# Performance work log

Measured on AMD Instinct MI355X. Metric: run time of the kernel, lower is better.

## Reference

```python
import jax, jax.numpy as jnp
import numpy as np

B, N, D, E_PER, NT, ET, L = 32, 64, 128, 512, 32, 16, 6
E = B * E_PER


def _ln(y, g, b, eps=1e-5):
    m = jnp.mean(y, -1, keepdims=True)
    v = jnp.mean((y - m) ** 2, -1, keepdims=True)
    return (y - m) * jax.lax.rsqrt(v + eps) * g + b


def setup_inputs() -> dict:
    key = jax.random.key(0)
    ks = jax.random.split(key, 40)
    x = jax.random.randint(ks[0], (B * N,), 0, NT)
    src = jax.random.randint(ks[1], (E,), 0, N)
    dst = jax.random.randint(ks[2], (E,), 0, N)
    off = jnp.repeat(jnp.arange(B) * N, E_PER)
    edge_index = jnp.stack([src + off, dst + off])
    edge_attr = jax.random.randint(ks[3], (E,), 0, ET)
    t = jax.random.uniform(ks[4], (B,))

    def lin(k, fi, fo):
        return jax.random.normal(k, (fi, fo), jnp.float32) / np.sqrt(fi).astype(np.float32)

    inp = {
        'x': x, 'edge_index': edge_index, 'edge_attr': edge_attr, 't': t,
        'node_emb': (jax.random.normal(ks[5], (NT, D)) * 0.02).at[0].set(0.0),
        'edge_emb': (jax.random.normal(ks[6], (ET, D)) * 0.02).at[0].set(0.0),
        'temb_W1': lin(ks[7], 1, D), 'temb_b1': jnp.zeros(D),
        'temb_W2': lin(ks[8], D, D), 'temb_b2': jnp.zeros(D),
        'nin_W1': lin(ks[9], D, 2 * D), 'nin_b1': jnp.zeros(2 * D),
        'nin_W2': lin(ks[10], 2 * D, D), 'nin_b2': jnp.zeros(D),
        'ein_W1': lin(ks[11], D, 2 * D), 'ein_b1': jnp.zeros(2 * D),
        'ein_W2': lin(ks[12], 2 * D, D), 'ein_b2': jnp.zeros(D),
        'conv_W1': jax.random.normal(ks[13], (L, 3 * D, D)) / np.sqrt(3 * D).astype(np.float32),
        'conv_b1': jnp.zeros((L, D)),
        'conv_g1': jnp.ones((L, D)), 'conv_bt1': jnp.zeros((L, D)),
        'conv_W2': jax.random.normal(ks[14], (L, D, D)) / np.sqrt(D).astype(np.float32),
        'conv_b2': jnp.zeros((L, D)),
        'conv_g2': jnp.ones((L, D)), 'conv_bt2': jnp.zeros((L, D)),
        'mlp_W1': lin(ks[15], D, D), 'mlp_b1': jnp.zeros(D),
        'mlp_W2': lin(ks[16], D, D), 'mlp_b2': jnp.zeros(D),
        'fn_W1': lin(ks[17], D, 2 * D), 'fn_b1': jnp.zeros(2 * D),
        'fn_W2': lin(ks[18], 2 * D, D), 'fn_b2': jnp.zeros(D),
    }
    return inp


def reference(x, edge_index, edge_attr, t, node_emb, edge_emb,
              temb_W1, temb_b1, temb_W2, temb_b2,
              nin_W1, nin_b1, nin_W2, nin_b2,
              ein_W1, ein_b1, ein_W2, ein_b2,
              conv_W1, conv_b1, conv_g1, conv_bt1,
              conv_W2, conv_b2, conv_g2, conv_bt2,
              mlp_W1, mlp_b1, mlp_W2, mlp_b2,
              fn_W1, fn_b1, fn_W2, fn_b2):
    silu, relu = jax.nn.silu, jax.nn.relu
    # encoders
    h = node_emb[x]                                   # (B*N, D)
    e = edge_emb[edge_attr]                           # (E, D)
    h = relu(h @ nin_W1 + nin_b1) @ nin_W2 + nin_b2
    e = relu(e @ ein_W1 + ein_b1) @ ein_W2 + ein_b2
    # densify (to_dense_adj sums duplicate edges)
    g = edge_index[0] // N
    u = edge_index[0] % N
    v = edge_index[1] % N
    adj = jnp.zeros((B, N, N, D), h.dtype).at[g, u, v].add(e)
    # time embedding scales adj
    tt = silu(silu(t[:, None] @ temb_W1 + temb_b1) @ temb_W2 + temb_b2)  # (B, D)
    X = adj * tt[:, None, None, :]
    A = X  # A fixed to initial masked tensor, X updated residually
    for l in range(L):
        X1 = jnp.einsum('bikd,bkjd->bijd', A, X)      # aggregate over dim 1
        X2 = jnp.einsum('bikd,bkjd->bijd', X, A)      # aggregate over dim 2
        y = jnp.concatenate([X, X1, X2], -1)          # (B,N,N,3D)
        y = relu(_ln(y @ conv_W1[l] + conv_b1[l], conv_g1[l], conv_bt1[l]))
        y = relu(_ln(y @ conv_W2[l] + conv_b2[l], conv_g2[l], conv_bt2[l]))
        X = X + y                                     # residual, samesparse add
    X = X + jnp.transpose(X, (0, 2, 1, 3))
    e_out = X[g, u, v]                                # (E, D) edge gather
    h2 = (silu(X @ mlp_W1 + mlp_b1) @ mlp_W2 + mlp_b2).mean(-2).reshape(B * N, D)
    node_out = relu(h2 @ fn_W1 + fn_b1) @ fn_W2 + fn_b2
    edge_out = relu(e_out @ fn_W1 + fn_b1) @ fn_W2 + fn_b2  # original uses final_layer_node for edges too
    graph_attr = node_out.reshape(B, N, -1).mean(1)   # global mean pool
    return node_out, edge_out, graph_attr
```

## Files before the change

### kernel.cpp

```cpp
#include <hip/hip_runtime.h>
#include <hip/hip_bf16.h>
#include <math.h>

#define NB 32
#define NNODE 64
#define DD 128
#define NSQ 4096
#define EDGES 16384
#define LAYERS 6

typedef __bf16 bf16x8 __attribute__((ext_vector_type(8)));
typedef float f32x4 __attribute__((ext_vector_type(4)));

typedef __attribute__((address_space(1))) const unsigned int g_u32;
typedef __attribute__((address_space(3))) unsigned int l_u32;
__device__ __forceinline__ void gll16(const void* g, void* l){
  __builtin_amdgcn_global_load_lds((g_u32*)g, (l_u32*)l, 16, 0, 0);
}

__device__ __forceinline__ float silu_f(float x){ return x / (1.f + __expf(-x)); }
__device__ __forceinline__ float bf2f(unsigned short h){
  union{unsigned int u; float f;} x; x.u = ((unsigned int)h)<<16; return x.f;
}

__global__ void k_temb(const float* __restrict__ t, const float* __restrict__ W1,
                       const float* __restrict__ b1, const float* __restrict__ W2,
                       const float* __restrict__ b2, float* __restrict__ tt){
  int b = blockIdx.x, d = threadIdx.x;
  __shared__ float h[DD];
  float v = t[b]*W1[d] + b1[d];
  h[d] = silu_f(v);
  __syncthreads();
  float acc = b2[d];
  #pragma unroll 4
  for (int k=0;k<DD;k++) acc = fmaf(h[k], W2[k*DD+d], acc);
  tt[b*DD+d] = silu_f(acc);
}

__global__ void k_edgeenc(const float* __restrict__ emb, const float* __restrict__ W1,
                          const float* __restrict__ b1, const float* __restrict__ W2,
                          const float* __restrict__ b2, float* __restrict__ enc){
  int et = blockIdx.x, tid = threadIdx.x;
  __shared__ float e0[DD];
  __shared__ float hid[2*DD];
  if (tid < DD) e0[tid] = emb[et*DD + tid];
  __syncthreads();
  float a = b1[tid];
  for (int d2=0; d2<DD; d2++) a = fmaf(e0[d2], W1[d2*256 + tid], a);
  hid[tid] = fmaxf(a, 0.f);
  __syncthreads();
  if (tid < DD){
    float o = b2[tid];
    for (int k=0;k<256;k++) o = fmaf(hid[k], W2[k*DD + tid], o);
    enc[et*DD + tid] = o;
  }
}

__global__ void k_cnt(const int* __restrict__ ei, const int* __restrict__ attr,
                      unsigned int* __restrict__ cnt, int b0){
  int e = b0*512 + blockIdx.x*256 + threadIdx.x;
  int s = ei[e], dN = ei[EDGES+e];
  int g = (s>>6) - b0, u = s&63, v = dN&63;
  atomicAdd(&cnt[((size_t)g*4096 + v*64 + u)*16 + attr[e]], 1u);
}

__global__ __launch_bounds__(256) void k_expand(const unsigned int* __restrict__ cnt,
    const float* __restrict__ enc, const float* __restrict__ tt,
    __bf16* __restrict__ A_S, int b0){
  __shared__ float encs[16][128];
  __shared__ float ttl[128];
  __shared__ __bf16 tb[8][256];
  int g = blockIdx.x >> 4;
  int cell0 = (blockIdx.x & 15) << 8;
  int tid = threadIdx.x;
  for (int s = tid; s < 2048; s += 256) encs[s>>7][s&127] = enc[s];
  if (tid < 128) ttl[tid] = tt[(b0+g)*128 + tid];
  unsigned int c16[16];
  { const uint4* src = (const uint4*)(cnt + ((size_t)g*4096 + cell0 + tid)*16);
    uint4 a = src[0], b = src[1], c = src[2], d = src[3];
    c16[0]=a.x; c16[1]=a.y; c16[2]=a.z; c16[3]=a.w;
    c16[4]=b.x; c16[5]=b.y; c16[6]=b.z; c16[7]=b.w;
    c16[8]=c.x; c16[9]=c.y; c16[10]=c.z; c16[11]=c.w;
    c16[12]=d.x; c16[13]=d.y; c16[14]=d.z; c16[15]=d.w; }
  __syncthreads();
  for (int dc=0; dc<16; dc++){
    int d0 = dc*8;
    float vals[8] = {0.f,0.f,0.f,0.f,0.f,0.f,0.f,0.f};
    #pragma unroll
    for (int et=0; et<16; et++){
      unsigned int c = c16[et];
      if (c){
        float fc = (float)c;
        #pragma unroll
        for (int dd=0; dd<8; dd++) vals[dd] = fmaf(fc, encs[et][d0+dd], vals[dd]);
      }
    }
    #pragma unroll
    for (int dd=0; dd<8; dd++) tb[dd][tid] = (__bf16)(vals[dd]*ttl[d0+dd]);
    __syncthreads();
    { int dd = tid>>5, seg = tid&31;
      uint4 v = *(const uint4*)&tb[dd][seg*8];
      *(uint4*)(A_S + ((size_t)(g*128 + d0 + dd)<<12) + cell0 + seg*8) = v; }
    __syncthreads();
  }
}

__global__ __launch_bounds__(256) void k_wprep(const float* __restrict__ W1, const float* __restrict__ W2,
                                               const float* __restrict__ Wm, __bf16* __restrict__ WT){
  int b = blockIdx.x, t = threadIdx.x;
  const float* src; __bf16* dst; int K;
  if (b < 6){ src = W1 + (size_t)b*384*128; dst = WT + (size_t)b*49152; K = 384; }
  else if (b < 12){ src = W2 + (size_t)(b-6)*128*128; dst = WT + 294912 + (size_t)(b-6)*16384; K = 128; }
  else { src = Wm; dst = WT + 393216; K = 128; }
  __shared__ float L[64][129];
  for (int k0 = 0; k0 < K; k0 += 64){
    __syncthreads();
    int r = t>>2, c = (t&3)*32;
    #pragma unroll
    for (int e=0;e<32;e+=4){
      float4 x = *(const float4*)(src + (size_t)(k0+r)*128 + c + e);
      L[r][c+e]=x.x; L[r][c+e+1]=x.y; L[r][c+e+2]=x.z; L[r][c+e+3]=x.w;
    }
    __syncthreads();
    int fo = t>>1, kk = (t&1)*32;
    union { __bf16 h[32]; uint4 u[4]; } o;
    #pragma unroll
    for (int e=0;e<32;e++) o.h[e] = (__bf16)L[kk+e][fo];
    uint4* d4 = (uint4*)(dst + (size_t)fo*K + k0 + kk);
    d4[0]=o.u[0]; d4[1]=o.u[1]; d4[2]=o.u[2]; d4[3]=o.u[3];
  }
}

__global__ __launch_bounds__(256) void k_wprepfn(const float* __restrict__ W1, const float* __restrict__ W2,
                                                 __bf16* __restrict__ o1, __bf16* __restrict__ o2){
  int b = blockIdx.x, t = threadIdx.x;
  const float* src; __bf16* dst; int K, N, k0, n0;
  if (b < 8){ src = W1; dst = o1; K = 128; N = 256; k0 = (b>>2)*64; n0 = (b&3)*64; }
  else { int bb = b-8; src = W2; dst = o2; K = 256; N = 128; k0 = (bb>>1)*64; n0 = (bb&1)*64; }
  __shared__ float L[64][65];
  int r = t>>2, c4 = (t&3)*16;
  #pragma unroll
  for (int e=0;e<16;e+=4){
    float4 x = *(const float4*)(src + (size_t)(k0+r)*N + n0 + c4 + e);
    L[r][c4+e]=x.x; L[r][c4+e+1]=x.y; L[r][c4+e+2]=x.z; L[r][c4+e+3]=x.w;
  }
  __syncthreads();
  int n = t>>2, kc = (t&3)*16;
  union { __bf16 h[16]; uint4 u[2]; } o;
  #pragma unroll
  for (int e=0;e<16;e++) o.h[e] = (__bf16)L[kc+e][n];
  uint4* d4 = (uint4*)(dst + (size_t)(n0+n)*K + k0 + kc);
  d4[0]=o.u[0]; d4[1]=o.u[1];
}

__global__ __launch_bounds__(256) void k_einsum(const __bf16* __restrict__ As,
                                                const __bf16* __restrict__ Xs,
                                                __bf16* __restrict__ X1t, __bf16* __restrict__ X2t){
  __shared__ __bf16 S[8][4096];
  int tid = threadIdx.x;
  int w = tid>>6, lane = tid&63;
  size_t p0 = (size_t)blockIdx.x * 2;
  {
    int slot = (w<2) ? (2+w) : (4+w);
    const __bf16* srcp = ((w<2) ? As : Xs) + (p0 + (w&1))*4096;
    #pragma unroll
    for (int c8 = 0; c8 < 8; c8++){
      int row = c8*8 + (lane>>3);
      int ch  = (lane&7) ^ (row&7);
      gll16(srcp + row*64 + ch*8, (char*)&S[slot][0] + c8*1024);
    }
  }
  __syncthreads();
  {
    int q = tid>>6, v = tid&63;
    int ssl = (q<2) ? (2+q) : (4+q);
    int dsl = (q<2) ? q : (2+q);
    const unsigned char* sb = (const unsigned char*)S[ssl];
    unsigned char* db = (unsigned char*)S[dsl];
    #pragma unroll
    for (int uo=0; uo<8; uo++){
      union { __bf16 h[8]; uint4 u; } pk;
      #pragma unroll
      for (int e=0;e<8;e++){
        int u = uo*8+e;
        pk.h[e] = *(const __bf16*)(sb + u*128 + (((v>>3) ^ (u&7))<<4) + (v&7)*2);
      }
      *(uint4*)(db + v*128 + ((uo ^ (v&7))<<4)) = pk.u;
    }
  }
  __syncthreads();
  int pl = w>>1, pr = w&1;
  const __bf16* M  = pr ? S[4+pl] : S[0+pl];
  const __bf16* Bt = pr ? S[2+pl] : S[6+pl];
  f32x4 acc[4][4];
  #pragma unroll
  for (int a=0;a<4;a++)
    #pragma unroll
    for(int b=0;b<4;b++) acc[a][b] = (f32x4){0.f,0.f,0.f,0.f};
  int lr = lane&15, lq = lane>>4;
  #pragma unroll
  for (int ks=0;ks<2;ks++){
    bf16x8 af[4], bfr[4];
    #pragma unroll
    for (int mt=0;mt<4;mt++){ int r = mt*16+lr; af[mt] = *(const bf16x8*)&M[r*64 + (((ks*4+lq) ^ (r&7))<<3)]; }
    #pragma unroll
    for (int nt=0;nt<4;nt++){ int r = nt*16+lr; bfr[nt] = *(const bf16x8*)&Bt[r*64 + (((ks*4+lq) ^ (r&7))<<3)]; }
    #pragma unroll
    for (int mt=0;mt<4;mt++)
      #pragma unroll
      for (int nt=0;nt<4;nt++)
        acc[mt][nt] = __builtin_amdgcn_mfma_f32_16x16x32_bf16(af[mt], bfr[nt], acc[mt][nt], 0,0,0);
  }
  {
    int dslot = pr ? (4+pl) : pl;
    unsigned char* db = (unsigned char*)&S[dslot][0];
    #pragma unroll
    for (int mt=0;mt<4;mt++)
      #pragma unroll
      for (int nt=0;nt<4;nt++){
        int col = nt*16 + lr; int row0 = mt*16 + lq*4;
        union { __bf16 h[4]; uint2 u; } o;
        #pragma unroll
        for (int r=0;r<4;r++) o.h[r] = (__bf16)acc[mt][nt][r];
        int chunk = row0>>3;
        *(uint2*)(db + col*128 + ((chunk ^ (col&7))<<4) + (row0&7)*2) = o.u;
      }
  }
  __syncthreads();
  #pragma unroll
  for (int s4=0; s4<4; s4++){
    int slot = (s4<2) ? s4 : (2+s4);
    __bf16* dst = ((s4<2) ? X1t : X2t) + (p0 + (s4&1))*4096;
    const unsigned char* sb = (const unsigned char*)&S[slot][0];
    #pragma unroll
    for (int q=0;q<2;q++){
      int t2 = tid + q*256;
      int col = t2>>3, rc = t2&7;
      uint4 v = *(const uint4*)(sb + col*128 + ((rc ^ (col&7))<<4));
      *(uint4*)(dst + t2*8) = v;
    }
  }
}

__global__ __launch_bounds__(256) void k_layer(const __bf16* __restrict__ Xold,
    const __bf16* __restrict__ X1, const __bf16* __restrict__ X2,
    const __bf16* __restrict__ W1t, const __bf16* __restrict__ W2t,
    const float* __restrict__ b1v, const float* __restrict__ g1v, const float* __restrict__ bt1v,
    const float* __restrict__ b2v, const float* __restrict__ g2v, const float* __restrict__ bt2v,
    __bf16* __restrict__ Xnew){
  __shared__ __align__(16) unsigned char WcB[8192];
  __shared__ __align__(16) unsigned char RG[32768];
  __bf16* Wc = (__bf16*)WcB;
  unsigned char* Nc = RG;
  unsigned char* Cc = RG + 8192;
  __bf16* y1T = (__bf16*)RG;
  float (*redS)[128] = (float(*)[128])(RG + 16384);
  float (*redQ)[128] = (float(*)[128])(RG + 18432);
  float (*stats)[128] = (float(*)[128])WcB;
  int tid = threadIdx.x, w = tid>>6, lane = tid&63, lr = lane&15, lq = lane>>4;
  int colTile = blockIdx.x << 7;
  int bl = colTile >> 12;
  int colInB = colTile & 4095;
  f32x4 acc[2][8];
  #pragma unroll
  for (int a=0;a<2;a++)
    #pragma unroll
    for (int b=0;b<8;b++) acc[a][b] = (f32x4){0.f,0.f,0.f,0.f};

  for (int ks=0; ks<12; ks++){
    __syncthreads();
    {
      #pragma unroll
      for (int cw=0; cw<2; cw++){
        int fo = (w*2+cw)*16 + (lane>>2);
        int c4 = lane&3;
        gll16(W1t + (size_t)fo*384 + ks*32 + ((c4 ^ (fo&3))<<3),
              (char*)WcB + (w*2+cw)*1024);
      }
    }
    {
      #pragma unroll
      for (int cn=0; cn<2; cn++){
        int fi = (w*2+cn)*4 + (lane>>4);
        int c16 = lane&15;
        int gfi = ks*32 + fi;
        const __bf16* T = (gfi<128)? Xold : (gfi<256? X1 : X2);
        int d = gfi & 127;
        gll16(T + ((size_t)(bl*128 + d)<<12) + colInB + ((c16 ^ (fi&15))<<3),
              (char*)RG + (w*2+cn)*1024);
      }
    }
    __syncthreads();
    {
      int col = tid>>1;
      #pragma unroll
      for (int j=0;j<2;j++){
        int oct = (tid&1)*2 + j;
        union { __bf16 h[8]; uint4 u; } pk;
        #pragma unroll
        for (int e=0;e<8;e++){
          int fi = oct*8 + e;
          pk.h[e] = *(const __bf16*)(Nc + fi*256 + (((col>>3) ^ (fi&15))<<4) + (col&7)*2);
        }
        *(uint4*)(Cc + col*64 + ((oct ^ (col&3))<<4)) = pk.u;
      }
    }
    __syncthreads();
    bf16x8 af[2], bfr[8];
    #pragma unroll
    for (int mt=0;mt<2;mt++){ int fo = w*32+mt*16+lr; af[mt] = *(const bf16x8*)&Wc[fo*32 + ((lq ^ (fo&3))<<3)]; }
    #pragma unroll
    for (int nt=0;nt<8;nt++){ int cr = nt*16+lr; bfr[nt] = *(const bf16x8*)(Cc + cr*64 + ((lq ^ (cr&3))<<4)); }
    #pragma unroll
    for (int mt=0;mt<2;mt++)
      #pragma unroll
      for (int nt=0;nt<8;nt++)
        acc[mt][nt] = __builtin_amdgcn_mfma_f32_16x16x32_bf16(af[mt], bfr[nt], acc[mt][nt], 0,0,0);
  }

  #pragma unroll
  for (int mt=0;mt<2;mt++){
    #pragma unroll
    for (int r=0;r<4;r++){
      float bv = b1v[w*32 + mt*16 + lq*4 + r];
      #pragma unroll
      for (int nt=0;nt<8;nt++) acc[mt][nt][r] += bv;
    }
  }
  {
    float cs[8], cq[8];
    #pragma unroll
    for (int nt=0;nt<8;nt++){ cs[nt]=0.f; cq[nt]=0.f; }
    #pragma unroll
    for (int mt=0;mt<2;mt++)
      #pragma unroll
      for (int nt=0;nt<8;nt++)
        #pragma unroll
        for (int r=0;r<4;r++){ float v = acc[mt][nt][r]; cs[nt] += v; cq[nt] = fmaf(v,v,cq[nt]); }
    #pragma unroll
    for (int nt=0;nt<8;nt++){
      cs[nt] += __shfl_xor(cs[nt], 16); cq[nt] += __shfl_xor(cq[nt], 16);
      cs[nt] += __shfl_xor(cs[nt], 32); cq[nt] += __shfl_xor(cq[nt], 32);
    }
    if (lq == 0){
      #pragma unroll
      for (int nt=0;nt<8;nt++){ redS[w][nt*16+lr] = cs[nt]; redQ[w][nt*16+lr] = cq[nt]; }
    }
  }
  __syncthreads();
  if (tid < 128){
    float S = redS[0][tid]+redS[1][tid]+redS[2][tid]+redS[3][tid];
    float Q = redQ[0][tid]+redQ[1][tid]+redQ[2][tid]+redQ[3][tid];
    float m = S*(1.f/128.f);
    float var = Q*(1.f/128.f) - m*m;
    stats[0][tid] = m; stats[1][tid] = rsqrtf(var + 1e-5f);
  }
  __syncthreads();
  #pragma unroll
  for (int mt=0;mt<2;mt++){
    int fo1b = w*32 + mt*16 + lq*4;
    float ga[4], be[4];
    #pragma unroll
    for (int r=0;r<4;r++){ ga[r] = g1v[fo1b+r]; be[r] = bt1v[fo1b+r]; }
    #pragma unroll
    for (int nt=0;nt<8;nt++){
      int col = nt*16 + lr;
      union { __bf16 h[4]; uint2 u; } o;
      #pragma unroll
      for (int r=0;r<4;r++){
        float xx = (acc[mt][nt][r] - stats[0][col]) * stats[1][col] * ga[r] + be[r];
        o.h[r] = (__bf16)fmaxf(xx, 0.f);
      }
      *(uint2*)&y1T[col*128 + (fo1b ^ ((col&15)<<3))] = o.u;
    }
  }
  __syncthreads();

  f32x4 acc2[2][8];
  #pragma unroll
  for (int a=0;a<2;a++)
    #pragma unroll
    for (int b=0;b<8;b++) acc2[a][b] = (f32x4){0.f,0.f,0.f,0.f};
  for (int ks2=0; ks2<4; ks2++){
    if (ks2) __syncthreads();
    {
      #pragma unroll
      for (int cw=0; cw<2; cw++){
        int fo = (w*2+cw)*16 + (lane>>2);
        int c4 = lane&3;
        gll16(W2t + (size_t)fo*128 + ks2*32 + ((c4 ^ (fo&3))<<3),
              (char*)WcB + (w*2+cw)*1024);
      }
    }
    __syncthreads();
    bf16x8 af[2], bfr[8];
    #pragma unroll
    for (int mt=0;mt<2;mt++){ int fo = w*32+mt*16+lr; af[mt] = *(const bf16x8*)&Wc[fo*32 + ((lq ^ (fo&3))<<3)]; }
    #pragma unroll
    for (int nt=0;nt<8;nt++){ int cr = nt*16+lr; bfr[nt] = *(const bf16x8*)&y1T[cr*128 + ((ks2*32 + lq*8) ^ ((cr&15)<<3))]; }
    #pragma unroll
    for (int mt=0;mt<2;mt++)
      #pragma unroll
      for (int nt=0;nt<8;nt++)
        acc2[mt][nt] = __builtin_amdgcn_mfma_f32_16x16x32_bf16(af[mt], bfr[nt], acc2[mt][nt], 0,0,0);
  }
  __syncthreads();

  #pragma unroll
  for (int mt=0;mt<2;mt++){
    #pragma unroll
    for (int r=0;r<4;r++){
      float bv = b2v[w*32 + mt*16 + lq*4 + r];
      #pragma unroll
      for (int nt=0;nt<8;nt++) acc2[mt][nt][r] += bv;
    }
  }
  {
    float cs[8], cq[8];
    #pragma unroll
    for (int nt=0;nt<8;nt++){ cs[nt]=0.f; cq[nt]=0.f; }
    #pragma unroll
    for (int mt=0;mt<2;mt++)
      #pragma unroll
      for (int nt=0;nt<8;nt++)
        #pragma unroll
        for (int r=0;r<4;r++){ float v = acc2[mt][nt][r]; cs[nt] += v; cq[nt] = fmaf(v,v,cq[nt]); }
    #pragma unroll
    for (int nt=0;nt<8;nt++){
      cs[nt] += __shfl_xor(cs[nt], 16); cq[nt] += __shfl_xor(cq[nt], 16);
      cs[nt] += __shfl_xor(cs[nt], 32); cq[nt] += __shfl_xor(cq[nt], 32);
    }
    if (lq == 0){
      #pragma unroll
      for (int nt=0;nt<8;nt++){ redS[w][nt*16+lr] = cs[nt]; redQ[w][nt*16+lr] = cq[nt]; }
    }
  }
  __syncthreads();
  if (tid < 128){
    float S = redS[0][tid]+redS[1][tid]+redS[2][tid]+redS[3][tid];
    float Q = redQ[0][tid]+redQ[1][tid]+redQ[2][tid]+redQ[3][tid];
    float m = S*(1.f/128.f);
    float var = Q*(1.f/128.f) - m*m;
    stats[0][tid] = m; stats[1][tid] = rsqrtf(var + 1e-5f);
  }
  __syncthreads();
  #pragma unroll
  for (int mt=0;mt<2;mt++){
    #pragma unroll
    for (int r=0;r<4;r++){
      int fo = w*32 + mt*16 + lq*4 + r;
      float ga = g2v[fo], be = bt2v[fo];
      #pragma unroll
      for (int nt=0;nt<8;nt++){
        int cp = nt*16 + lr;
        float xx = (acc2[mt][nt][r] - stats[0][cp]) * stats[1][cp] * ga + be;
        int ch = cp>>3;
        int swz = (ch & 8) | ((ch ^ (fo&7)) & 7);
        *(__bf16*)(RG + fo*256 + (swz<<4) + (cp&7)*2) = (__bf16)fmaxf(xx, 0.f);
      }
    }
  }
  __syncthreads();
  {
    int row = tid>>1, half = tid&1;
    size_t gb = ((size_t)(bl*128 + row)<<12) + colInB + half*64;
    #pragma unroll
    for (int j=0;j<8;j++){
      int ch = half*8 + j;
      int swz = (ch & 8) | ((ch ^ (row&7)) & 7);
      uint4 tv = *(const uint4*)(RG + row*256 + (swz<<4));
      uint4 ov = *(const uint4*)(Xold + gb + j*8);
      union { __bf16 h[8]; uint4 u; } a, b, o;
      a.u = tv; b.u = ov;
      #pragma unroll
      for (int e=0;e<8;e++) o.h[e] = (__bf16)((float)a.h[e] + (float)b.h[e]);
      *(uint4*)(Xnew + gb + j*8) = o.u;
    }
  }
}

__global__ __launch_bounds__(256) void k_sym(const __bf16* __restrict__ Xin, __bf16* __restrict__ Xout){
  __shared__ float P[64][65];
  size_t base = (size_t)blockIdx.x * 4096;
  int tid = threadIdx.x;
  int f = tid*16, r = f>>6, c = f&63;
  union { __bf16 h[16]; uint4 u[2]; } in;
  in.u[0] = *(const uint4*)(Xin + base + f);
  in.u[1] = *(const uint4*)(Xin + base + f + 8);
  #pragma unroll
  for (int e=0;e<16;e++) P[r][c+e] = (float)in.h[e];
  __syncthreads();
  union { __bf16 h[16]; uint4 u[2]; } o;
  #pragma unroll
  for (int e=0;e<16;e++) o.h[e] = (__bf16)(P[r][c+e] + P[c+e][r]);
  *(uint4*)(Xout + base + f)     = o.u[0];
  *(uint4*)(Xout + base + f + 8) = o.u[1];
}

__global__ __launch_bounds__(256) void k_tonm(const __bf16* __restrict__ S, __bf16* __restrict__ NM){
  __shared__ unsigned short L[64][65];
  int b = blockIdx.x;
  int g = b >> 7, dh = (b>>6)&1, cc = b&63;
  int cell0 = cc*64, d0 = dh*64;
  int tid = threadIdx.x;
  int r = tid>>2, c = (tid&3)*16;
  union { unsigned short h[16]; uint4 u[2]; } in;
  const unsigned short* src = (const unsigned short*)S + ((size_t)(g*128 + d0 + r)<<12) + cell0 + c;
  in.u[0] = *(const uint4*)src;
  in.u[1] = *(const uint4*)(src + 8);
  #pragma unroll
  for (int e=0;e<16;e++) L[r][c+e] = in.h[e];
  __syncthreads();
  union { unsigned short h[16]; uint4 u[2]; } o;
  int cr = tid>>2, dc = (tid&3)*16;
  #pragma unroll
  for (int e=0;e<16;e++) o.h[e] = L[dc+e][cr];
  unsigned short* dst = (unsigned short*)NM + (size_t)(g*4096 + cell0 + cr)*128 + d0 + dc;
  *(uint4*)dst       = o.u[0];
  *(uint4*)(dst + 8) = o.u[1];
}

__global__ __launch_bounds__(256) void k_mlph(const __bf16* __restrict__ NM,
    const __bf16* __restrict__ Wt, const float* __restrict__ bias, __bf16* __restrict__ hid){
  __shared__ __align__(16) unsigned char WcB[8192];
  __shared__ __align__(16) unsigned char EcB[8192];
  __bf16* Wc = (__bf16*)WcB;
  unsigned char* Ec = EcB;
  int tid = threadIdx.x, w = tid>>6, lane = tid&63, lr = lane&15, lq = lane>>4;
  int g = blockIdx.x >> 5;
  size_t cellbase = ((size_t)g<<12) + ((size_t)(blockIdx.x & 31) << 7);
  int mh = w&1, nh = w>>1;
  f32x4 acc[4][4];
  #pragma unroll
  for (int a=0;a<4;a++)
    #pragma unroll
    for (int b=0;b<4;b++) acc[a][b] = (f32x4){0.f,0.f,0.f,0.f};
  for (int ks=0; ks<4; ks++){
    __syncthreads();
    { int fo = tid>>1, half = tid&1;
      const uint4* src = (const uint4*)(Wt + (size_t)fo*128 + ks*32 + half*16);
      uint4 v0 = src[0], v1 = src[1];
      *(uint4*)&Wc[fo*32 + (((half*2+0) ^ (fo&3))<<3)] = v0;
      *(uint4*)&Wc[fo*32 + (((half*2+1) ^ (fo&3))<<3)] = v1;
    }
    { int cell = tid>>1, half = tid&1;
      const uint4* src = (const uint4*)(NM + (cellbase + cell)*128 + ks*32 + half*16);
      uint4 v0 = src[0], v1 = src[1];
      *(uint4*)(Ec + cell*64 + (((half*2+0) ^ (cell&3))<<4)) = v0;
      *(uint4*)(Ec + cell*64 + (((half*2+1) ^ (cell&3))<<4)) = v1;
    }
    __syncthreads();
    bf16x8 af[4], bfr[4];
    #pragma unroll
    for (int mt=0;mt<4;mt++){ int cr = mh*64 + mt*16 + lr; af[mt] = *(const bf16x8*)(Ec + cr*64 + ((lq ^ (cr&3))<<4)); }
    #pragma unroll
    for (int nt=0;nt<4;nt++){ int fo = nh*64 + nt*16 + lr; bfr[nt] = *(const bf16x8*)&Wc[fo*32 + ((lq ^ (fo&3))<<3)]; }
    #pragma unroll
    for (int mt=0;mt<4;mt++)
      #pragma unroll
      for (int nt=0;nt<4;nt++)
        acc[mt][nt] = __builtin_amdgcn_mfma_f32_16x16x32_bf16(af[mt], bfr[nt], acc[mt][nt], 0,0,0);
  }
  #pragma unroll
  for (int mt=0;mt<4;mt++)
    #pragma unroll
    for (int r=0;r<4;r++){
      size_t cell = cellbase + mh*64 + mt*16 + lq*4 + r;
      #pragma unroll
      for (int nt=0;nt<4;nt++){
        int fo = nh*64 + nt*16 + lr;
        hid[cell*128 + fo] = (__bf16)silu_f(acc[mt][nt][r] + bias[fo]);
      }
    }
}

__global__ void k_ymean(const __bf16* __restrict__ hid, float* __restrict__ ym){
  __shared__ float red[256];
  int g = blockIdx.x >> 6, u = blockIdx.x & 63;
  int fo = threadIdx.x & 127, vh = threadIdx.x >> 7;
  const unsigned short* hu = (const unsigned short*)hid;
  float s = 0.f;
  for (int v = vh; v < 64; v += 2)
    s += bf2f(hu[((size_t)g*4096 + v*64 + u)*128 + fo]);
  red[threadIdx.x] = s;
  __syncthreads();
  if (vh == 0) ym[((size_t)g*64 + u)*128 + fo] = (red[fo] + red[128+fo]) * (1.f/64.f);
}

__global__ void k_h2(const float* __restrict__ ym, const float* __restrict__ W2,
                     const float* __restrict__ b2, float* __restrict__ h2){
  int row = blockIdx.x, fo = threadIdx.x;
  __shared__ float rr[128];
  rr[fo] = ym[(size_t)row*128 + fo];
  __syncthreads();
  float a = b2[fo];
  #pragma unroll 4
  for (int k=0;k<128;k++) a = fmaf(rr[k], W2[k*128+fo], a);
  h2[(size_t)row*128+fo] = a;
}

template<int GATHER>
__global__ __launch_bounds__(256) void k_fmlp(const __bf16* __restrict__ NM, const float* __restrict__ RWS,
    const int* __restrict__ ei,
    const __bf16* __restrict__ W1t, const float* __restrict__ b1,
    const __bf16* __restrict__ W2t, const float* __restrict__ b2,
    float* __restrict__ outp, int b0){
  __shared__ __align__(16) unsigned char RA[32768];
  __shared__ __align__(16) unsigned char RB[8192];
  __shared__ int cells[64];
  __bf16* eo  = (__bf16*)RA;
  __bf16* Wc  = (__bf16*)(RA + 16384);
  __bf16* hid = (__bf16*)RA;
  __bf16* W2c = (__bf16*)RB;
  int tid = threadIdx.x, w = tid>>6, lane = tid&63, lr = lane&15, lq = lane>>4;
  int r0 = blockIdx.x*64;
  if (GATHER){
    if (tid < 64){
      int e = b0*512 + r0 + tid;
      int s = ei[e], dN = ei[EDGES+e];
      cells[tid] = ((s>>6) - b0)*4096 + (dN&63)*64 + (s&63);
    }
    __syncthreads();
  }
  { int el = tid>>2, o4 = tid&3;
    if (GATHER){
      const unsigned short* src = (const unsigned short*)NM + (size_t)cells[el]*128;
      #pragma unroll
      for (int j=0;j<4;j++){
        int ch = o4*4 + j;
        uint4 v = *(const uint4*)(src + ch*8);
        *(uint4*)&eo[el*128 + ((ch*8) ^ ((el&15)*8))] = v;
      }
    } else {
      const float* src = RWS + (size_t)(r0 + el)*128;
      #pragma unroll
      for (int j=0;j<4;j++){
        int ch = o4*4 + j;
        union { __bf16 h[8]; uint4 u; } pk;
        #pragma unroll
        for (int e2=0;e2<8;e2++) pk.h[e2] = (__bf16)src[ch*8 + e2];
        *(uint4*)&eo[el*128 + ((ch*8) ^ ((el&15)*8))] = pk.u;
      }
    }
  }
  f32x4 acc[4][4];
  #pragma unroll
  for (int a=0;a<4;a++)
    #pragma unroll
    for (int b=0;b<4;b++) acc[a][b] = (f32x4){0.f,0.f,0.f,0.f};
  for (int ks=0; ks<4; ks++){
    if (ks) __syncthreads();
    { int fo = tid;
      const uint4* src = (const uint4*)(W1t + (size_t)fo*128 + ks*32);
      #pragma unroll
      for (int o=0;o<4;o++){
        uint4 v = src[o];
        *(uint4*)&Wc[fo*32 + ((o ^ (fo&3))<<3)] = v;
      }
    }
    __syncthreads();
    bf16x8 af[4], bfr[4];
    #pragma unroll
    for (int mt=0;mt<4;mt++){ int fo = w*64+mt*16+lr; af[mt] = *(const bf16x8*)&Wc[fo*32 + ((lq ^ (fo&3))<<3)]; }
    #pragma unroll
    for (int nt=0;nt<4;nt++){ int ed = nt*16+lr; bfr[nt] = *(const bf16x8*)&eo[ed*128 + ((ks*32+lq*8) ^ ((ed&15)*8))]; }
    #pragma unroll
    for (int mt=0;mt<4;mt++)
      #pragma unroll
      for (int nt=0;nt<4;nt++)
        acc[mt][nt] = __builtin_amdgcn_mfma_f32_16x16x32_bf16(af[mt], bfr[nt], acc[mt][nt], 0,0,0);
  }
  __syncthreads();
  #pragma unroll
  for (int mt=0;mt<4;mt++){
    int fob = w*64 + mt*16 + lq*4;
    float bv[4];
    #pragma unroll
    for (int r=0;r<4;r++) bv[r] = b1[fob+r];
    #pragma unroll
    for (int nt=0;nt<4;nt++){
      int ed = nt*16 + lr;
      union { __bf16 h[4]; uint2 u; } o;
      #pragma unroll
      for (int r=0;r<4;r++) o.h[r] = (__bf16)fmaxf(acc[mt][nt][r] + bv[r], 0.f);
      *(uint2*)&hid[ed*256 + (fob ^ ((ed&31)*8))] = o.u;
    }
  }
  f32x4 acc2[4][2];
  #pragma unroll
  for (int a=0;a<4;a++)
    #pragma unroll
    for (int b=0;b<2;b++) acc2[a][b] = (f32x4){0.f,0.f,0.f,0.f};
  int mh = w&1, nh = w>>1;
  for (int ks2=0; ks2<8; ks2++){
    __syncthreads();
    { int fo = tid>>1, half = tid&1;
      const uint4* src = (const uint4*)(W2t + (size_t)fo*256 + ks2*32 + half*16);
      uint4 v0 = src[0], v1 = src[1];
      *(uint4*)&W2c[fo*32 + (((half*2+0) ^ (fo&3))<<3)] = v0;
      *(uint4*)&W2c[fo*32 + (((half*2+1) ^ (fo&3))<<3)] = v1;
    }
    __syncthreads();
    bf16x8 af2[4], bfr2[2];
    #pragma unroll
    for (int mt=0;mt<4;mt++){ int fo2 = mh*64+mt*16+lr; af2[mt] = *(const bf16x8*)&W2c[fo2*32 + ((lq ^ (fo2&3))<<3)]; }
    #pragma unroll
    for (int nt=0;nt<2;nt++){ int ed = nh*32+nt*16+lr; bfr2[nt] = *(const bf16x8*)&hid[ed*256 + ((ks2*32+lq*8) ^ ((ed&31)*8))]; }
    #pragma unroll
    for (int mt=0;mt<4;mt++)
      #pragma unroll
      for (int nt=0;nt<2;nt++)
        acc2[mt][nt] = __builtin_amdgcn_mfma_f32_16x16x32_bf16(af2[mt], bfr2[nt], acc2[mt][nt], 0,0,0);
  }
  #pragma unroll
  for (int mt=0;mt<4;mt++){
    int fo2b = mh*64 + mt*16 + lq*4;
    float bv[4];
    #pragma unroll
    for (int r=0;r<4;r++) bv[r] = b2[fo2b+r];
    #pragma unroll
    for (int nt=0;nt<2;nt++){
      int ed = nh*32 + nt*16 + lr;
      float4 o = make_float4(acc2[mt][nt][0]+bv[0], acc2[mt][nt][1]+bv[1],
                             acc2[mt][nt][2]+bv[2], acc2[mt][nt][3]+bv[3]);
      *(float4*)(outp + (size_t)(r0 + ed)*128 + fo2b) = o;
    }
  }
}

__global__ void k_graph(const float* __restrict__ node_out, float* __restrict__ gout){
  int b = blockIdx.x, d = threadIdx.x;
  float s = 0.f;
  for (int i=0;i<64;i++) s += node_out[(size_t)(b*64+i)*128 + d];
  gout[b*128 + d] = s * (1.f/64.f);
}

extern "C" void kernel_launch(void* const* d_in, const int* in_sizes, int n_in,
                              void* d_out, int out_size, void* d_ws, size_t ws_size,
                              hipStream_t stream) {
  const int*   edge_index = (const int*)d_in[1];
  const int*   edge_attr  = (const int*)d_in[2];
  const float* t        = (const float*)d_in[3];
  const float* edge_emb = (const float*)d_in[5];
  const float* temb_W1  = (const float*)d_in[6];
  const float* temb_b1  = (const float*)d_in[7];
  const float* temb_W2  = (const float*)d_in[8];
  const float* temb_b2  = (const float*)d_in[9];
  const float* ein_W1   = (const float*)d_in[14];
  const float* ein_b1   = (const float*)d_in[15];
  const float* ein_W2   = (const float*)d_in[16];
  const float* ein_b2   = (const float*)d_in[17];
  const float* conv_W1  = (const float*)d_in[18];
  const float* conv_b1  = (const float*)d_in[19];
  const float* conv_g1  = (const float*)d_in[20];
  const float* conv_bt1 = (const float*)d_in[21];
  const float* conv_W2  = (const float*)d_in[22];
  const float* conv_b2  = (const float*)d_in[23];
  const float* conv_g2  = (const float*)d_in[24];
  const float* conv_bt2 = (const float*)d_in[25];
  const float* mlp_W1   = (const float*)d_in[26];
  const float* mlp_b1   = (const float*)d_in[27];
  const float* mlp_W2   = (const float*)d_in[28];
  const float* mlp_b2   = (const float*)d_in[29];
  const float* fn_W1    = (const float*)d_in[30];
  const float* fn_b1    = (const float*)d_in[31];
  const float* fn_W2    = (const float*)d_in[32];
  const float* fn_b2    = (const float*)d_in[33];

  float* ws  = (float*)d_ws;
  float* tt  = ws;
  float* enc = ws + 4096;
  float* ym  = ws + 6144;
  float* h2  = ws + 268288;
  __bf16* WT = (__bf16*)(ws + 530432);
  unsigned int* cnt = (unsigned int*)(ws + 768000);
  const size_t HDRF = 2883584;

  __bf16* fnW1t = WT + 409600;
  __bf16* fnW2t = WT + 442368;

  size_t availF = ws_size / sizeof(float);
  const int cands[6] = {32, 16, 8, 4, 2, 1};
  int C = 1;
  for (int i = 0; i < 6; i++){
    if (HDRF + 4ull * (size_t)cands[i] * 262144ull <= availF){ C = cands[i]; break; }
  }
  const size_t PCB = (size_t)C * 262144;
  __bf16* A_S = (__bf16*)(ws + HDRF);
  __bf16* X_S = (__bf16*)(ws + HDRF + PCB);
  __bf16* X1  = (__bf16*)(ws + HDRF + 2*PCB);
  __bf16* X2  = (__bf16*)(ws + HDRF + 3*PCB);
  float* outf = (float*)d_out;

  k_temb<<<NB, DD, 0, stream>>>(t, temb_W1, temb_b1, temb_W2, temb_b2, tt);
  k_edgeenc<<<16, 256, 0, stream>>>(edge_emb, ein_W1, ein_b1, ein_W2, ein_b2, enc);
  k_wprep<<<13, 256, 0, stream>>>(conv_W1, conv_W2, mlp_W1, WT);
  k_wprepfn<<<16, 256, 0, stream>>>(fn_W1, fn_W2, fnW1t, fnW2t);

  for (int b0 = 0; b0 < NB; b0 += C){
    hipMemsetAsync(cnt, 0, (size_t)C*4096*16*sizeof(unsigned int), stream);
    k_cnt<<<C*2, 256, 0, stream>>>(edge_index, edge_attr, cnt, b0);
    k_expand<<<C*16, 256, 0, stream>>>(cnt, enc, tt, A_S, b0);

    for (int l=0; l<LAYERS; l++){
      const __bf16* Xs_l = (l==0) ? A_S : X_S;
      k_einsum<<<C*64, 256, 0, stream>>>(A_S, Xs_l, X1, X2);
      k_layer<<<C*32, 256, 0, stream>>>(Xs_l, X1, X2,
          WT + (size_t)l*49152, WT + 294912 + (size_t)l*16384,
          conv_b1 + l*DD, conv_g1 + l*DD, conv_bt1 + l*DD,
          conv_b2 + l*DD, conv_g2 + l*DD, conv_bt2 + l*DD, X_S);
    }

    k_sym<<<C*128, 256, 0, stream>>>(X_S, X2);
    k_tonm<<<C*128, 256, 0, stream>>>(X2, X1);
    k_mlph<<<C*32, 256, 0, stream>>>(X1, WT + 393216, mlp_b1, X2);
    k_ymean<<<C*64, 256, 0, stream>>>(X2, ym);
    k_h2<<<C*64, 128, 0, stream>>>(ym, mlp_W2, mlp_b2, h2);
    k_fmlp<1><<<C*8, 256, 0, stream>>>(X1, nullptr, edge_index, fnW1t, fn_b1, fnW2t, fn_b2,
                                       outf + 262144 + (size_t)b0*512*128, b0);
    k_fmlp<0><<<C, 256, 0, stream>>>(nullptr, h2, nullptr, fnW1t, fn_b1, fnW2t, fn_b2,
                                     outf + (size_t)b0*64*128, b0);
    k_graph<<<C, DD, 0, stream>>>(outf + (size_t)b0*64*DD, outf + 2359296 + b0*DD);
  }
}
```

Measured before the change: 645.8 us.

## Prefetch next activation slice in registers and read layer weights directly from global

```diff
diff --git a/kernel.cpp b/kernel.cpp
--- a/kernel.cpp
+++ b/kernel.cpp
@@ -248,51 +248,37 @@
     const float* __restrict__ b1v, const float* __restrict__ g1v, const float* __restrict__ bt1v,
     const float* __restrict__ b2v, const float* __restrict__ g2v, const float* __restrict__ bt2v,
     __bf16* __restrict__ Xnew){
-  __shared__ __align__(16) unsigned char WcB[8192];
   __shared__ __align__(16) unsigned char RG[32768];
-  __bf16* Wc = (__bf16*)WcB;
+  __shared__ float stats[2][128];
   unsigned char* Nc = RG;
   unsigned char* Cc = RG + 8192;
   __bf16* y1T = (__bf16*)RG;
   float (*redS)[128] = (float(*)[128])(RG + 16384);
   float (*redQ)[128] = (float(*)[128])(RG + 18432);
-  float (*stats)[128] = (float(*)[128])WcB;
   int tid = threadIdx.x, w = tid>>6, lane = tid&63, lr = lane&15, lq = lane>>4;
   int colTile = blockIdx.x << 7;
   int bl = colTile >> 12;
   int colInB = colTile & 4095;
+  int s_fi = tid>>3, s_o = tid&7;
+
   f32x4 acc[2][8];
   #pragma unroll
   for (int a=0;a<2;a++)
     #pragma unroll
     for (int b=0;b<8;b++) acc[a][b] = (f32x4){0.f,0.f,0.f,0.f};
 
+  {
+    int gfi = s_fi;
+    const __bf16* T = Xold;
+    const uint4* src = (const uint4*)(T + ((size_t)(bl*128 + gfi)<<12) + colInB + s_o*16);
+    uint4 v0 = src[0], v1 = src[1];
+    *(uint4*)(Nc + s_fi*256 + (((s_o*2+0) ^ (s_fi&15))<<4)) = v0;
+    *(uint4*)(Nc + s_fi*256 + (((s_o*2+1) ^ (s_fi&15))<<4)) = v1;
+  }
+  __syncthreads();
+
   for (int ks=0; ks<12; ks++){
-    __syncthreads();
-    {
-      #pragma unroll
-      for (int cw=0; cw<2; cw++){
-        int fo = (w*2+cw)*16 + (lane>>2);
-        int c4 = lane&3;
-        gll16(W1t + (size_t)fo*384 + ks*32 + ((c4 ^ (fo&3))<<3),
-              (char*)WcB + (w*2+cw)*1024);
-      }
-    }
-    {
-      #pragma unroll
-      for (int cn=0; cn<2; cn++){
-        int fi = (w*2+cn)*4 + (lane>>4);
-        int c16 = lane&15;
-        int gfi = ks*32 + fi;
-        const __bf16* T = (gfi<128)? Xold : (gfi<256? X1 : X2);
-        int d = gfi & 127;
-        gll16(T + ((size_t)(bl*128 + d)<<12) + colInB + ((c16 ^ (fi&15))<<3),
-              (char*)RG + (w*2+cn)*1024);
-      }
-    }
-    __syncthreads();
-    {
-      int col = tid>>1;
+    { int col = tid>>1;
       #pragma unroll
       for (int j=0;j<2;j++){
         int oct = (tid&1)*2 + j;
@@ -306,9 +292,22 @@
       }
     }
     __syncthreads();
-    bf16x8 af[2], bfr[8];
-    #pragma unroll
-    for (int mt=0;mt<2;mt++){ int fo = w*32+mt*16+lr; af[mt] = *(const bf16x8*)&Wc[fo*32 + ((lq ^ (fo&3))<<3)]; }
+    if (ks < 11){
+      int gfi = (ks+1)*32 + s_fi;
+      const __bf16* T = (gfi<128)? Xold : (gfi<256? X1 : X2);
+      int d = gfi & 127;
+      const uint4* src = (const uint4*)(T + ((size_t)(bl*128 + d)<<12) + colInB + s_o*16);
+      uint4 v0 = src[0], v1 = src[1];
+      *(uint4*)(Nc + s_fi*256 + (((s_o*2+0) ^ (s_fi&15))<<4)) = v0;
+      *(uint4*)(Nc + s_fi*256 + (((s_o*2+1) ^ (s_fi&15))<<4)) = v1;
+    }
+    bf16x8 af[2];
+    #pragma unroll
+    for (int mt=0;mt<2;mt++){
+      int fo = w*32 + mt*16 + lr;
+      af[mt] = *(const bf16x8*)(W1t + (size_t)fo*384 + ks*32 + lq*8);
+    }
+    bf16x8 bfr[8];
     #pragma unroll
     for (int nt=0;nt<8;nt++){ int cr = nt*16+lr; bfr[nt] = *(const bf16x8*)(Cc + cr*64 + ((lq ^ (cr&3))<<4)); }
     #pragma unroll
@@ -316,6 +315,7 @@
       #pragma unroll
       for (int nt=0;nt<8;nt++)
         acc[mt][nt] = __builtin_amdgcn_mfma_f32_16x16x32_bf16(af[mt], bfr[nt], acc[mt][nt], 0,0,0);
+    __syncthreads();
   }
 
   #pragma unroll
@@ -381,21 +381,14 @@
   for (int a=0;a<2;a++)
     #pragma unroll
     for (int b=0;b<8;b++) acc2[a][b] = (f32x4){0.f,0.f,0.f,0.f};
+  #pragma unroll
   for (int ks2=0; ks2<4; ks2++){
-    if (ks2) __syncthreads();
-    {
-      #pragma unroll
-      for (int cw=0; cw<2; cw++){
-        int fo = (w*2+cw)*16 + (lane>>2);
-        int c4 = lane&3;
-        gll16(W2t + (size_t)fo*128 + ks2*32 + ((c4 ^ (fo&3))<<3),
-              (char*)WcB + (w*2+cw)*1024);
-      }
-    }
-    __syncthreads();
     bf16x8 af[2], bfr[8];
     #pragma unroll
-    for (int mt=0;mt<2;mt++){ int fo = w*32+mt*16+lr; af[mt] = *(const bf16x8*)&Wc[fo*32 + ((lq ^ (fo&3))<<3)]; }
+    for (int mt=0;mt<2;mt++){
+      int fo = w*32 + mt*16 + lr;
+      af[mt] = *(const bf16x8*)(W2t + (size_t)fo*128 + ks2*32 + lq*8);
+    }
     #pragma unroll
     for (int nt=0;nt<8;nt++){ int cr = nt*16+lr; bfr[nt] = *(const bf16x8*)&y1T[cr*128 + ((ks2*32 + lq*8) ^ ((cr&15)<<3))]; }
     #pragma unroll
@@ -450,31 +443,15 @@
     for (int r=0;r<4;r++){
       int fo = w*32 + mt*16 + lq*4 + r;
       float ga = g2v[fo], be = bt2v[fo];
+      size_t rowb = ((size_t)(bl*128 + fo)<<12) + colInB;
       #pragma unroll
       for (int nt=0;nt<8;nt++){
         int cp = nt*16 + lr;
         float xx = (acc2[mt][nt][r] - stats[0][cp]) * stats[1][cp] * ga + be;
-        int ch = cp>>3;
-        int swz = (ch & 8) | ((ch ^ (fo&7)) & 7);
-        *(__bf16*)(RG + fo*256 + (swz<<4) + (cp&7)*2) = (__bf16)fmaxf(xx, 0.f);
-      }
-    }
-  }
-  __syncthreads();
-  {
-    int row = tid>>1, half = tid&1;
-    size_t gb = ((size_t)(bl*128 + row)<<12) + colInB + half*64;
-    #pragma unroll
-    for (int j=0;j<8;j++){
-      int ch = half*8 + j;
-      int swz = (ch & 8) | ((ch ^ (row&7)) & 7);
-      uint4 tv = *(const uint4*)(RG + row*256 + (swz<<4));
-      uint4 ov = *(const uint4*)(Xold + gb + j*8);
-      union { __bf16 h[8]; uint4 u; } a, b, o;
-      a.u = tv; b.u = ov;
-      #pragma unroll
-      for (int e=0;e<8;e++) o.h[e] = (__bf16)((float)a.h[e] + (float)b.h[e]);
-      *(uint4*)(Xnew + gb + j*8) = o.u;
+        float o = fmaxf(xx, 0.f);
+        float old = (float)Xold[rowb + cp];
+        Xnew[rowb + cp] = (__bf16)(o + old);
+      }
     }
   }
 }
```

New measurement: 599.2 us. 7.2% less time.
